# Kernel tuning notes

Measured on AMD Instinct MI355X. Metric: run time of the kernel, lower is better.

Reference implementation:

```python
import math
import jax, jax.numpy as jnp
import numpy as np

B, L, H = 8, 2048, 256


def setup_inputs() -> dict:
    key = jax.random.key(0)
    k1, k2, k3, k4, k5 = jax.random.split(key, 5)
    inputs = jax.random.normal(k1, (B, L, H), dtype=jnp.float32)
    scale = 1.0 / math.sqrt(H)
    Wq = jax.random.normal(k2, (H, H), dtype=jnp.float32) * scale
    Wk = jax.random.normal(k3, (H, H), dtype=jnp.float32) * scale
    Wv = jax.random.normal(k4, (H, H), dtype=jnp.float32) * scale
    lens = jax.random.randint(k5, (B,), L // 2, L + 1)
    lens = lens.at[0].set(L)  # original assumes max(lens) == L
    return {"inputs": inputs, "Wq": Wq, "Wk": Wk, "Wv": Wv, "lens": lens}


def reference(inputs, Wq, Wk, Wv, lens):
    # nn.Linear(bias=False): y = x @ W.T
    Q = jnp.einsum('blh,oh->blo', inputs, Wq)
    K = jnp.einsum('blh,oh->blo', inputs, Wk)
    V = jnp.einsum('blh,oh->blo', inputs, Wv)
    d = Q.shape[-1]
    alpha = jnp.einsum('bqd,bkd->bqk', Q, K) / math.sqrt(d)  # [B, L, L]
    # key-padding mask: [B, 1, L] broadcast over query dim (matches expand)
    mask = (jnp.arange(L)[None, :] < lens[:, None])[:, None, :]
    NEG = jnp.float32(-2.0 ** 31)
    alpha = jnp.where(mask, alpha, NEG)
    alpha = jax.nn.softmax(alpha, axis=2)
    out = jnp.einsum('bqk,bkd->bqd', alpha, V)
    return out
```

## Files before the change

### kernel.cpp

```cpp
#include <hip/hip_runtime.h>

#define BB 8
#define LL 2048
#define DD 256

typedef _Float16 half8 __attribute__((ext_vector_type(8)));
typedef float floatx4 __attribute__((ext_vector_type(4)));
typedef unsigned short ushort8 __attribute__((ext_vector_type(8)));

__device__ inline unsigned short f2h(float f) {
  _Float16 h = (_Float16)f;
  return __builtin_bit_cast(unsigned short, h);
}

__global__ __launch_bounds__(256) void wcvt(
    const float* __restrict__ Wq, const float* __restrict__ Wk,
    const float* __restrict__ Wv, unsigned short* __restrict__ Wh) {
  const int bm = blockIdx.x >> 5;
  const float* src = (bm == 0) ? Wq : (bm == 1) ? Wk : Wv;
  const int off = (blockIdx.x & 31) * 2048 + threadIdx.x * 8;
  float4 a = *(const float4*)(src + off);
  float4 b = *(const float4*)(src + off + 4);
  ushort8 u = {f2h(a.x), f2h(a.y), f2h(a.z), f2h(a.w),
               f2h(b.x), f2h(b.y), f2h(b.z), f2h(b.w)};
  *(ushort8*)(Wh + bm * 65536 + off) = u;
}

__global__ __launch_bounds__(256) void proj(
    const float* __restrict__ x, const unsigned short* __restrict__ Wh,
    unsigned short* __restrict__ Qb, unsigned short* __restrict__ Kb,
    unsigned short* __restrict__ VT) {
  __shared__ __attribute__((aligned(16))) unsigned short tile[10240];
  const int t = threadIdx.x;
  const int wave = t >> 6, lane = t & 63, quad = lane >> 4, m16 = lane & 15;
  const int l0g = blockIdx.x * 32;
  const int b = l0g >> 11, lb = l0g & 2047;

  half8 xf[2][8];
  for (int mt = 0; mt < 2; ++mt) {
    const float* xp = x + (size_t)(l0g + mt * 16 + m16) * DD + quad * 8;
    for (int kb = 0; kb < 8; ++kb) {
      float4 a = *(const float4*)(xp + kb * 32);
      float4 c = *(const float4*)(xp + kb * 32 + 4);
      ushort8 u = {f2h(a.x), f2h(a.y), f2h(a.z), f2h(a.w),
                   f2h(c.x), f2h(c.y), f2h(c.z), f2h(c.w)};
      xf[mt][kb] = __builtin_bit_cast(half8, u);
    }
  }

  for (int mat = 0; mat < 3; ++mat) {
    for (int j = 0; j < 4; ++j) {
      const int ot = wave * 4 + j;
      const unsigned short* wp =
          Wh + mat * 65536 + (ot * 16 + m16) * DD + quad * 8;
      floatx4 acc[2] = {{0, 0, 0, 0}, {0, 0, 0, 0}};
      if (mat < 2) {
        for (int kb = 0; kb < 8; ++kb) {
          half8 wf =
              __builtin_bit_cast(half8, *(const ushort8*)(wp + kb * 32));
          acc[0] = __builtin_amdgcn_mfma_f32_16x16x32_f16(xf[0][kb], wf,
                                                          acc[0], 0, 0, 0);
          acc[1] = __builtin_amdgcn_mfma_f32_16x16x32_f16(xf[1][kb], wf,
                                                          acc[1], 0, 0, 0);
        }
        for (int mt = 0; mt < 2; ++mt)
          for (int r = 0; r < 4; ++r)
            tile[(mt * 16 + quad * 4 + r) * 264 + ot * 16 + m16] =
                f2h(acc[mt][r]);
      } else {
        for (int kb = 0; kb < 8; ++kb) {
          half8 wf =
              __builtin_bit_cast(half8, *(const ushort8*)(wp + kb * 32));
          acc[0] = __builtin_amdgcn_mfma_f32_16x16x32_f16(wf, xf[0][kb],
                                                          acc[0], 0, 0, 0);
          acc[1] = __builtin_amdgcn_mfma_f32_16x16x32_f16(wf, xf[1][kb],
                                                          acc[1], 0, 0, 0);
        }
        for (int mt = 0; mt < 2; ++mt)
          for (int r = 0; r < 4; ++r)
            tile[(ot * 16 + quad * 4 + r) * 40 + mt * 16 + m16] =
                f2h(acc[mt][r]);
      }
    }
    __syncthreads();
    if (mat < 2) {
      unsigned short* Out = mat ? Kb : Qb;
      const int row = t >> 3, c0 = (t & 7) * 8;
      for (int i = 0; i < 4; ++i) {
        ushort8 v = *(const ushort8*)&tile[row * 264 + c0 + i * 64];
        *(ushort8*)(Out + (size_t)(l0g + row) * DD + c0 + i * 64) = v;
      }
    } else {
      const int dd = t >> 2, lc = (t & 3) * 8;
      for (int p = 0; p < 4; ++p) {
        const int d = p * 64 + dd;
        ushort8 v = *(const ushort8*)&tile[d * 40 + lc];
        *(ushort8*)(VT + ((size_t)(b * DD + d)) * LL + lb + lc) = v;
      }
    }
    __syncthreads();
  }
}

__global__ __launch_bounds__(512, 2) void attn(
    const unsigned short* __restrict__ Qb, const unsigned short* __restrict__ Kb,
    const unsigned short* __restrict__ VT, const int* __restrict__ lens,
    float* __restrict__ out) {
  __shared__ __attribute__((aligned(16))) unsigned char smem[149504];
  const int t = threadIdx.x;
  const int wave = t >> 6, lane = t & 63, quad = lane >> 4, m16 = lane & 15;
  const int grp = wave >> 2, qw = wave & 3, tgl = t & 255;
  unsigned short* Ks = (unsigned short*)(smem + grp * 32768);
  unsigned short* Vs = (unsigned short*)(smem + 65536 + grp * 32768);
  unsigned short* Pw = (unsigned short*)(smem + 131072 + wave * 2304);

  const int b = blockIdx.x;
  const int q0 = blockIdx.y * 64;
  const int len = lens[b];
  const size_t baseQK = (size_t)b * LL * DD;
  const size_t baseVT = (size_t)b * DD * LL;

  half8 qf[8];
  {
    const unsigned short* qrow =
        Qb + baseQK + (size_t)(q0 + qw * 16 + m16) * DD + quad * 8;
    for (int kb = 0; kb < 8; ++kb)
      qf[kb] = __builtin_bit_cast(half8, *(const ushort8*)(qrow + kb * 32));
  }

  floatx4 O[16];
  for (int i = 0; i < 16; ++i) O[i] = (floatx4){0, 0, 0, 0};
  float mrow[4] = {-1e30f, -1e30f, -1e30f, -1e30f};
  float lrow[4] = {0.f, 0.f, 0.f, 0.f};

  ushort8 kreg[8], vreg[8];
  const unsigned short* kbase = Kb + baseQK;
  const unsigned short* vbase = VT + baseVT;

#define LOAD_TILES(KV0)                                                      \
  {                                                                          \
    const unsigned short* kp = kbase + (size_t)(KV0)*DD;                     \
    for (int c = 0; c < 8; ++c)                                              \
      kreg[c] = *(const ushort8*)(kp + (tgl + c * 256) * 8);                 \
    for (int c = 0; c < 8; ++c) {                                            \
      int ch = tgl + c * 256;                                                \
      vreg[c] = *(const ushort8*)(vbase + (size_t)(ch >> 3) * LL + (KV0) +   \
                                  (ch & 7) * 8);                             \
    }                                                                        \
  }

  const int T = (len + 127) >> 7;
  LOAD_TILES(grp * 64);
  asm volatile("" ::: "memory");

  for (int it = 0; it < T; ++it) {
    const int kv0 = it * 128 + grp * 64;
    __syncthreads();
    for (int c = 0; c < 8; ++c) {
      int ch = tgl + c * 256, row = ch >> 5, cc = ch & 31;
      *(ushort8*)&Ks[row * 256 + (cc ^ (row & 7)) * 8] = kreg[c];
    }
    for (int c = 0; c < 8; ++c) {
      int ch = tgl + c * 256, d = ch >> 3, cc = ch & 7;
      *(ushort8*)&Vs[d * 64 + (cc ^ (d & 7)) * 8] = vreg[c];
    }
    __syncthreads();
    if (it + 1 < T) {
      LOAD_TILES(kv0 + 128);
      asm volatile("" ::: "memory");
    }

    if (kv0 < len) {
      floatx4 s[4];
      for (int n = 0; n < 4; ++n) s[n] = (floatx4){0, 0, 0, 0};
      __builtin_amdgcn_s_setprio(1);
      for (int kb = 0; kb < 8; ++kb)
        for (int n = 0; n < 4; ++n) {
          half8 kf = __builtin_bit_cast(
              half8, *(const ushort8*)&Ks[(n * 16 + m16) * 256 +
                                          (((kb * 4 + quad) ^ (m16 & 7)) * 8)]);
          s[n] = __builtin_amdgcn_mfma_f32_16x16x32_f16(qf[kb], kf, s[n], 0, 0, 0);
        }
      __builtin_amdgcn_s_setprio(0);
      float sv[4][4];
      for (int n = 0; n < 4; ++n) {
        bool valid = (kv0 + n * 16 + m16) < len;
        for (int r = 0; r < 4; ++r)
          sv[n][r] = valid ? s[n][r] * 0.0625f : -1e30f;
      }
      float al[4];
      for (int r = 0; r < 4; ++r) {
        float v = fmaxf(fmaxf(sv[0][r], sv[1][r]), fmaxf(sv[2][r], sv[3][r]));
        v = fmaxf(v, __shfl_xor(v, 1));
        v = fmaxf(v, __shfl_xor(v, 2));
        v = fmaxf(v, __shfl_xor(v, 4));
        v = fmaxf(v, __shfl_xor(v, 8));
        float mn = fmaxf(mrow[r], v);
        al[r] = __expf(mrow[r] - mn);
        mrow[r] = mn;
        float sum = 0.f;
        for (int n = 0; n < 4; ++n) {
          float p = __expf(sv[n][r] - mn);
          Pw[(quad * 4 + r) * 72 + n * 16 + m16] = f2h(p);
          sum += p;
        }
        sum += __shfl_xor(sum, 1);
        sum += __shfl_xor(sum, 2);
        sum += __shfl_xor(sum, 4);
        sum += __shfl_xor(sum, 8);
        lrow[r] = lrow[r] * al[r] + sum;
      }
      for (int i = 0; i < 16; ++i)
        for (int r = 0; r < 4; ++r) O[i][r] *= al[r];
      half8 pf0 = __builtin_bit_cast(half8,
                                     *(const ushort8*)&Pw[m16 * 72 + quad * 8]);
      half8 pf1 = __builtin_bit_cast(
          half8, *(const ushort8*)&Pw[m16 * 72 + 32 + quad * 8]);
      __builtin_amdgcn_s_setprio(1);
      for (int nb = 0; nb < 16; ++nb) {
        half8 vf0 = __builtin_bit_cast(
            half8, *(const ushort8*)&Vs[(nb * 16 + m16) * 64 +
                                        ((quad ^ (m16 & 7)) * 8)]);
        O[nb] = __builtin_amdgcn_mfma_f32_16x16x32_f16(pf0, vf0, O[nb], 0, 0, 0);
        half8 vf1 = __builtin_bit_cast(
            half8, *(const ushort8*)&Vs[(nb * 16 + m16) * 64 +
                                        (((4 + quad) ^ (m16 & 7)) * 8)]);
        O[nb] = __builtin_amdgcn_mfma_f32_16x16x32_f16(pf1, vf1, O[nb], 0, 0, 0);
      }
      __builtin_amdgcn_s_setprio(0);
    }
  }
#undef LOAD_TILES

  __syncthreads();
  float* Om = (float*)(smem) + qw * 4112;
  float* ml = (float*)(smem + 65792) + qw * 32;
  if (grp == 1) {
    for (int nb = 0; nb < 16; ++nb)
      for (int r = 0; r < 4; ++r)
        Om[(quad * 4 + r) * 257 + nb * 16 + m16] = O[nb][r];
    if (m16 == 0)
      for (int r = 0; r < 4; ++r) {
        ml[(quad * 4 + r) * 2] = mrow[r];
        ml[(quad * 4 + r) * 2 + 1] = lrow[r];
      }
  }
  __syncthreads();
  if (grp == 0) {
    float a[4], bf[4], inv[4];
    for (int r = 0; r < 4; ++r) {
      float mB = ml[(quad * 4 + r) * 2];
      float lB = ml[(quad * 4 + r) * 2 + 1];
      float m = fmaxf(mrow[r], mB);
      a[r] = __expf(mrow[r] - m);
      bf[r] = __expf(mB - m);
      inv[r] = 1.f / (lrow[r] * a[r] + lB * bf[r]);
    }
    for (int nb = 0; nb < 16; ++nb)
      for (int r = 0; r < 4; ++r) {
        float ob = Om[(quad * 4 + r) * 257 + nb * 16 + m16];
        out[baseQK + (size_t)(q0 + qw * 16 + quad * 4 + r) * DD + nb * 16 +
            m16] = (O[nb][r] * a[r] + ob * bf[r]) * inv[r];
      }
  }
}

extern "C" void kernel_launch(void* const* d_in, const int* in_sizes, int n_in,
                              void* d_out, int out_size, void* d_ws, size_t ws_size,
                              hipStream_t stream) {
  const float* x = (const float*)d_in[0];
  const float* Wq = (const float*)d_in[1];
  const float* Wk = (const float*)d_in[2];
  const float* Wv = (const float*)d_in[3];
  const int* lens = (const int*)d_in[4];
  unsigned short* Qb = (unsigned short*)d_ws;
  unsigned short* Kb = Qb + (size_t)BB * LL * DD;
  unsigned short* VT = Kb + (size_t)BB * LL * DD;
  unsigned short* Wh = VT + (size_t)BB * LL * DD;
  float* out = (float*)d_out;

  wcvt<<<96, 256, 0, stream>>>(Wq, Wk, Wv, Wh);
  proj<<<512, 256, 0, stream>>>(x, Wh, Qb, Kb, VT);
  attn<<<dim3(8, 32), 512, 0, stream>>>(Qb, Kb, VT, lens, out);
}
```

Baseline: 182.6 us.

## Restructure attention waves to share K/V fragments across two query tiles with direct-to-LDS loads

```diff
diff --git a/kernel.cpp b/kernel.cpp
--- a/kernel.cpp
+++ b/kernel.cpp
@@ -12,6 +12,11 @@
   _Float16 h = (_Float16)f;
   return __builtin_bit_cast(unsigned short, h);
 }
+
+#define GLD16(src, ldsbase)                                                    \
+  __builtin_amdgcn_global_load_lds(                                           \
+      (const __attribute__((address_space(1))) unsigned int*)(src),           \
+      (__attribute__((address_space(3))) unsigned int*)(ldsbase), 16, 0, 0)
 
 __global__ __launch_bounds__(256) void wcvt(
     const float* __restrict__ Wq, const float* __restrict__ Wk,
@@ -106,162 +111,230 @@
     const unsigned short* __restrict__ Qb, const unsigned short* __restrict__ Kb,
     const unsigned short* __restrict__ VT, const int* __restrict__ lens,
     float* __restrict__ out) {
-  __shared__ __attribute__((aligned(16))) unsigned char smem[149504];
+  __shared__ __attribute__((aligned(16))) unsigned char smem[151552];
   const int t = threadIdx.x;
   const int wave = t >> 6, lane = t & 63, quad = lane >> 4, m16 = lane & 15;
-  const int grp = wave >> 2, qw = wave & 3, tgl = t & 255;
-  unsigned short* Ks = (unsigned short*)(smem + grp * 32768);
-  unsigned short* Vs = (unsigned short*)(smem + 65536 + grp * 32768);
-  unsigned short* Pw = (unsigned short*)(smem + 131072 + wave * 2304);
+  const int qw = wave >> 2, grp = wave & 3;
+  unsigned short* Ks = (unsigned short*)(smem + grp * 16384);
+  unsigned short* Vs = (unsigned short*)(smem + 65536 + grp * 16384);
+  unsigned short* Pw = (unsigned short*)(smem + 131072 + wave * 2560);
 
   const int b = blockIdx.x;
-  const int q0 = blockIdx.y * 64;
+  const int q0 = blockIdx.y * 64 + qw * 32;
   const int len = lens[b];
   const size_t baseQK = (size_t)b * LL * DD;
   const size_t baseVT = (size_t)b * DD * LL;
-
-  half8 qf[8];
-  {
-    const unsigned short* qrow =
-        Qb + baseQK + (size_t)(q0 + qw * 16 + m16) * DD + quad * 8;
-    for (int kb = 0; kb < 8; ++kb)
-      qf[kb] = __builtin_bit_cast(half8, *(const ushort8*)(qrow + kb * 32));
-  }
-
-  floatx4 O[16];
-  for (int i = 0; i < 16; ++i) O[i] = (floatx4){0, 0, 0, 0};
-  float mrow[4] = {-1e30f, -1e30f, -1e30f, -1e30f};
-  float lrow[4] = {0.f, 0.f, 0.f, 0.f};
-
-  ushort8 kreg[8], vreg[8];
   const unsigned short* kbase = Kb + baseQK;
   const unsigned short* vbase = VT + baseVT;
 
-#define LOAD_TILES(KV0)                                                      \
-  {                                                                          \
-    const unsigned short* kp = kbase + (size_t)(KV0)*DD;                     \
-    for (int c = 0; c < 8; ++c)                                              \
-      kreg[c] = *(const ushort8*)(kp + (tgl + c * 256) * 8);                 \
-    for (int c = 0; c < 8; ++c) {                                            \
-      int ch = tgl + c * 256;                                                \
-      vreg[c] = *(const ushort8*)(vbase + (size_t)(ch >> 3) * LL + (KV0) +   \
-                                  (ch & 7) * 8);                             \
-    }                                                                        \
+  half8 qf[2][8];
+  for (int mt = 0; mt < 2; ++mt) {
+    const unsigned short* qrow =
+        Qb + baseQK + (size_t)(q0 + mt * 16 + m16) * DD + quad * 8;
+    for (int kb = 0; kb < 8; ++kb)
+      qf[mt][kb] = __builtin_bit_cast(half8, *(const ushort8*)(qrow + kb * 32));
+  }
+
+  floatx4 O[2][16];
+  for (int mt = 0; mt < 2; ++mt)
+    for (int i = 0; i < 16; ++i) O[mt][i] = (floatx4){0, 0, 0, 0};
+  float mrow[2][4], lrow[2][4];
+  for (int mt = 0; mt < 2; ++mt)
+    for (int r = 0; r < 4; ++r) {
+      mrow[mt][r] = -1e30f;
+      lrow[mt][r] = 0.f;
+    }
+
+#define STAGE_K(KV0)                                                          \
+  for (int c = 0; c < 8; ++c) {                                               \
+    int idx = c * 512 + t;                                                    \
+    int gs = idx >> 10, ch = idx & 1023, row = ch >> 5, cc = ch & 31;         \
+    const unsigned short* src = kbase +                                       \
+        (size_t)((KV0) + gs * 32 + row) * DD + ((cc ^ (row & 7)) << 3);       \
+    GLD16(src, smem + (c * 512 + wave * 64) * 16);                            \
+  }
+#define STAGE_V(KV0)                                                          \
+  for (int c = 0; c < 8; ++c) {                                               \
+    int idx = c * 512 + t;                                                    \
+    int gs = idx >> 10, ch = idx & 1023, d = ch >> 2, cv = ch & 3;            \
+    const unsigned short* src = vbase + (size_t)d * LL + (KV0) + gs * 32 +    \
+                                ((cv ^ ((d >> 1) & 3)) << 3);                 \
+    GLD16(src, smem + 65536 + (c * 512 + wave * 64) * 16);                    \
   }
 
   const int T = (len + 127) >> 7;
-  LOAD_TILES(grp * 64);
-  asm volatile("" ::: "memory");
+  STAGE_K(0);
+  STAGE_V(0);
+  __syncthreads();
 
   for (int it = 0; it < T; ++it) {
-    const int kv0 = it * 128 + grp * 64;
-    __syncthreads();
-    for (int c = 0; c < 8; ++c) {
-      int ch = tgl + c * 256, row = ch >> 5, cc = ch & 31;
-      *(ushort8*)&Ks[row * 256 + (cc ^ (row & 7)) * 8] = kreg[c];
-    }
-    for (int c = 0; c < 8; ++c) {
-      int ch = tgl + c * 256, d = ch >> 3, cc = ch & 7;
-      *(ushort8*)&Vs[d * 64 + (cc ^ (d & 7)) * 8] = vreg[c];
-    }
-    __syncthreads();
-    if (it + 1 < T) {
-      LOAD_TILES(kv0 + 128);
-      asm volatile("" ::: "memory");
-    }
-
-    if (kv0 < len) {
-      floatx4 s[4];
-      for (int n = 0; n < 4; ++n) s[n] = (floatx4){0, 0, 0, 0};
+    const int kv0 = it * 128;
+    const int kvg = kv0 + grp * 32;
+    const bool active = kvg < len;
+    const bool more = (it + 1) < T;
+
+    floatx4 s[2][2];
+    if (active) {
+      for (int mt = 0; mt < 2; ++mt)
+        for (int n = 0; n < 2; ++n) s[mt][n] = (floatx4){0, 0, 0, 0};
       __builtin_amdgcn_s_setprio(1);
       for (int kb = 0; kb < 8; ++kb)
-        for (int n = 0; n < 4; ++n) {
+        for (int n = 0; n < 2; ++n) {
           half8 kf = __builtin_bit_cast(
               half8, *(const ushort8*)&Ks[(n * 16 + m16) * 256 +
-                                          (((kb * 4 + quad) ^ (m16 & 7)) * 8)]);
-          s[n] = __builtin_amdgcn_mfma_f32_16x16x32_f16(qf[kb], kf, s[n], 0, 0, 0);
+                                          (((kb * 4 + quad) ^ (m16 & 7)) << 3)]);
+          s[0][n] = __builtin_amdgcn_mfma_f32_16x16x32_f16(qf[0][kb], kf,
+                                                           s[0][n], 0, 0, 0);
+          s[1][n] = __builtin_amdgcn_mfma_f32_16x16x32_f16(qf[1][kb], kf,
+                                                           s[1][n], 0, 0, 0);
         }
       __builtin_amdgcn_s_setprio(0);
-      float sv[4][4];
-      for (int n = 0; n < 4; ++n) {
-        bool valid = (kv0 + n * 16 + m16) < len;
-        for (int r = 0; r < 4; ++r)
-          sv[n][r] = valid ? s[n][r] * 0.0625f : -1e30f;
-      }
-      float al[4];
-      for (int r = 0; r < 4; ++r) {
-        float v = fmaxf(fmaxf(sv[0][r], sv[1][r]), fmaxf(sv[2][r], sv[3][r]));
-        v = fmaxf(v, __shfl_xor(v, 1));
-        v = fmaxf(v, __shfl_xor(v, 2));
-        v = fmaxf(v, __shfl_xor(v, 4));
-        v = fmaxf(v, __shfl_xor(v, 8));
-        float mn = fmaxf(mrow[r], v);
-        al[r] = __expf(mrow[r] - mn);
-        mrow[r] = mn;
-        float sum = 0.f;
-        for (int n = 0; n < 4; ++n) {
-          float p = __expf(sv[n][r] - mn);
-          Pw[(quad * 4 + r) * 72 + n * 16 + m16] = f2h(p);
-          sum += p;
-        }
-        sum += __shfl_xor(sum, 1);
-        sum += __shfl_xor(sum, 2);
-        sum += __shfl_xor(sum, 4);
-        sum += __shfl_xor(sum, 8);
-        lrow[r] = lrow[r] * al[r] + sum;
-      }
-      for (int i = 0; i < 16; ++i)
-        for (int r = 0; r < 4; ++r) O[i][r] *= al[r];
-      half8 pf0 = __builtin_bit_cast(half8,
-                                     *(const ushort8*)&Pw[m16 * 72 + quad * 8]);
-      half8 pf1 = __builtin_bit_cast(
-          half8, *(const ushort8*)&Pw[m16 * 72 + 32 + quad * 8]);
+    }
+    __syncthreads();
+    if (more) STAGE_K(kv0 + 128);
+
+    if (active) {
+      float sv[2][2][4];
+      bool vld[2];
+      for (int n = 0; n < 2; ++n) vld[n] = (kvg + n * 16 + m16) < len;
+      for (int mt = 0; mt < 2; ++mt)
+        for (int n = 0; n < 2; ++n)
+          for (int r = 0; r < 4; ++r)
+            sv[mt][n][r] = vld[n] ? s[mt][n][r] * 0.0625f : -1e30f;
+      float alv[2][4];
+      for (int mt = 0; mt < 2; ++mt)
+        for (int r = 0; r < 4; ++r) {
+          float v = fmaxf(sv[mt][0][r], sv[mt][1][r]);
+          v = fmaxf(v, __shfl_xor(v, 1));
+          v = fmaxf(v, __shfl_xor(v, 2));
+          v = fmaxf(v, __shfl_xor(v, 4));
+          v = fmaxf(v, __shfl_xor(v, 8));
+          float mn = fmaxf(mrow[mt][r], v);
+          float al = __expf(mrow[mt][r] - mn);
+          mrow[mt][r] = mn;
+          float sum = 0.f;
+          for (int n = 0; n < 2; ++n) {
+            float p = __expf(sv[mt][n][r] - mn);
+            Pw[(mt * 16 + quad * 4 + r) * 40 + n * 16 + m16] = f2h(p);
+            sum += p;
+          }
+          sum += __shfl_xor(sum, 1);
+          sum += __shfl_xor(sum, 2);
+          sum += __shfl_xor(sum, 4);
+          sum += __shfl_xor(sum, 8);
+          lrow[mt][r] = lrow[mt][r] * al + sum;
+          alv[mt][r] = al;
+        }
+      for (int mt = 0; mt < 2; ++mt)
+        for (int nb = 0; nb < 16; ++nb)
+          for (int r = 0; r < 4; ++r) O[mt][nb][r] *= alv[mt][r];
+      half8 pf[2];
+      for (int mt = 0; mt < 2; ++mt)
+        pf[mt] = __builtin_bit_cast(
+            half8, *(const ushort8*)&Pw[(mt * 16 + m16) * 40 + quad * 8]);
       __builtin_amdgcn_s_setprio(1);
       for (int nb = 0; nb < 16; ++nb) {
-        half8 vf0 = __builtin_bit_cast(
-            half8, *(const ushort8*)&Vs[(nb * 16 + m16) * 64 +
-                                        ((quad ^ (m16 & 7)) * 8)]);
-        O[nb] = __builtin_amdgcn_mfma_f32_16x16x32_f16(pf0, vf0, O[nb], 0, 0, 0);
-        half8 vf1 = __builtin_bit_cast(
-            half8, *(const ushort8*)&Vs[(nb * 16 + m16) * 64 +
-                                        (((4 + quad) ^ (m16 & 7)) * 8)]);
-        O[nb] = __builtin_amdgcn_mfma_f32_16x16x32_f16(pf1, vf1, O[nb], 0, 0, 0);
+        const int d = nb * 16 + m16;
+        half8 vf = __builtin_bit_cast(
+            half8,
+            *(const ushort8*)&Vs[d * 32 + ((quad ^ ((d >> 1) & 3)) << 3)]);
+        O[0][nb] = __builtin_amdgcn_mfma_f32_16x16x32_f16(pf[0], vf, O[0][nb],
+                                                          0, 0, 0);
+        O[1][nb] = __builtin_amdgcn_mfma_f32_16x16x32_f16(pf[1], vf, O[1][nb],
+                                                          0, 0, 0);
       }
       __builtin_amdgcn_s_setprio(0);
     }
-  }
-#undef LOAD_TILES
-
-  __syncthreads();
-  float* Om = (float*)(smem) + qw * 4112;
-  float* ml = (float*)(smem + 65792) + qw * 32;
+    __syncthreads();
+    if (more) STAGE_V(kv0 + 128);
+    __syncthreads();
+  }
+#undef STAGE_K
+#undef STAGE_V
+
+  __syncthreads();
+  float* OmB = (float*)smem;
+  float* mlB = (float*)(smem + 131584);
+  if (grp >= 2) {
+    const int slot = (grp & 1) + 2 * qw;
+    float* Om = OmB + slot * 8224;
+    float* ml = mlB + slot * 64;
+    for (int mt = 0; mt < 2; ++mt)
+      for (int nb = 0; nb < 16; ++nb)
+        for (int r = 0; r < 4; ++r)
+          Om[(mt * 16 + quad * 4 + r) * 257 + nb * 16 + m16] = O[mt][nb][r];
+    if (m16 == 0)
+      for (int mt = 0; mt < 2; ++mt)
+        for (int r = 0; r < 4; ++r) {
+          ml[(mt * 16 + quad * 4 + r) * 2] = mrow[mt][r];
+          ml[(mt * 16 + quad * 4 + r) * 2 + 1] = lrow[mt][r];
+        }
+  }
+  __syncthreads();
+  if (grp < 2) {
+    const int slot = grp + 2 * qw;
+    float* Om = OmB + slot * 8224;
+    float* ml = mlB + slot * 64;
+    float av[2][4], bv[2][4];
+    for (int mt = 0; mt < 2; ++mt)
+      for (int r = 0; r < 4; ++r) {
+        const int row = mt * 16 + quad * 4 + r;
+        float mB = ml[row * 2], lB = ml[row * 2 + 1];
+        float m = fmaxf(mrow[mt][r], mB);
+        float a = __expf(mrow[mt][r] - m);
+        float bb = __expf(mB - m);
+        lrow[mt][r] = lrow[mt][r] * a + lB * bb;
+        mrow[mt][r] = m;
+        av[mt][r] = a;
+        bv[mt][r] = bb;
+      }
+    for (int mt = 0; mt < 2; ++mt)
+      for (int nb = 0; nb < 16; ++nb)
+        for (int r = 0; r < 4; ++r)
+          O[mt][nb][r] =
+              O[mt][nb][r] * av[mt][r] +
+              Om[(mt * 16 + quad * 4 + r) * 257 + nb * 16 + m16] * bv[mt][r];
+  }
+  __syncthreads();
   if (grp == 1) {
-    for (int nb = 0; nb < 16; ++nb)
-      for (int r = 0; r < 4; ++r)
-        Om[(quad * 4 + r) * 257 + nb * 16 + m16] = O[nb][r];
+    const int slot = qw;
+    float* Om = OmB + slot * 8224;
+    float* ml = mlB + slot * 64;
+    for (int mt = 0; mt < 2; ++mt)
+      for (int nb = 0; nb < 16; ++nb)
+        for (int r = 0; r < 4; ++r)
+          Om[(mt * 16 + quad * 4 + r) * 257 + nb * 16 + m16] = O[mt][nb][r];
     if (m16 == 0)
+      for (int mt = 0; mt < 2; ++mt)
+        for (int r = 0; r < 4; ++r) {
+          ml[(mt * 16 + quad * 4 + r) * 2] = mrow[mt][r];
+          ml[(mt * 16 + quad * 4 + r) * 2 + 1] = lrow[mt][r];
+        }
+  }
+  __syncthreads();
+  if (grp == 0) {
+    const int slot = qw;
+    float* Om = OmB + slot * 8224;
+    float* ml = mlB + slot * 64;
+    float av[2][4], bv[2][4], inv[2][4];
+    for (int mt = 0; mt < 2; ++mt)
       for (int r = 0; r < 4; ++r) {
-        ml[(quad * 4 + r) * 2] = mrow[r];
-        ml[(quad * 4 + r) * 2 + 1] = lrow[r];
-      }
-  }
-  __syncthreads();
-  if (grp == 0) {
-    float a[4], bf[4], inv[4];
-    for (int r = 0; r < 4; ++r) {
-      float mB = ml[(quad * 4 + r) * 2];
-      float lB = ml[(quad * 4 + r) * 2 + 1];
-      float m = fmaxf(mrow[r], mB);
-      a[r] = __expf(mrow[r] - m);
-      bf[r] = __expf(mB - m);
-      inv[r] = 1.f / (lrow[r] * a[r] + lB * bf[r]);
-    }
-    for (int nb = 0; nb < 16; ++nb)
-      for (int r = 0; r < 4; ++r) {
-        float ob = Om[(quad * 4 + r) * 257 + nb * 16 + m16];
-        out[baseQK + (size_t)(q0 + qw * 16 + quad * 4 + r) * DD + nb * 16 +
-            m16] = (O[nb][r] * a[r] + ob * bf[r]) * inv[r];
-      }
+        const int row = mt * 16 + quad * 4 + r;
+        float mB = ml[row * 2], lB = ml[row * 2 + 1];
+        float m = fmaxf(mrow[mt][r], mB);
+        float a = __expf(mrow[mt][r] - m);
+        float bb = __expf(mB - m);
+        av[mt][r] = a;
+        bv[mt][r] = bb;
+        inv[mt][r] = 1.f / (lrow[mt][r] * a + lB * bb);
+      }
+    for (int mt = 0; mt < 2; ++mt)
+      for (int nb = 0; nb < 16; ++nb)
+        for (int r = 0; r < 4; ++r) {
+          float ob = Om[(mt * 16 + quad * 4 + r) * 257 + nb * 16 + m16];
+          out[baseQK + (size_t)(q0 + mt * 16 + quad * 4 + r) * DD + nb * 16 +
+              m16] = (O[mt][nb][r] * av[mt][r] + ob * bv[mt][r]) * inv[mt][r];
+        }
   }
 }
 
```

After: 233.0 us. 1.28x slower.
